# Performance work log

Measured on AMD Instinct MI355X. Metric: run time of the kernel, lower is better.

Reference implementation:

```python
import jax, jax.numpy as jnp
import numpy as np

B, T, D, H = 8, 4096, 1024, 1024


def setup_inputs() -> dict:
    key = jax.random.key(0)
    ks = jax.random.split(key, 8)
    s = 1.0 / np.sqrt(D)
    x = jax.random.normal(ks[0], (B, T, D), dtype=jnp.float32)
    Wq = jax.random.uniform(ks[1], (H, D), jnp.float32, -s, s)
    bq = jax.random.uniform(ks[2], (H,), jnp.float32, -s, s)
    Wk = jax.random.uniform(ks[3], (H, D), jnp.float32, -s, s)
    bk = jax.random.uniform(ks[4], (H,), jnp.float32, -s, s)
    Wv = jax.random.uniform(ks[5], (H, D), jnp.float32, -s, s)
    bv = jax.random.uniform(ks[6], (H,), jnp.float32, -s, s)
    wbias = jax.random.uniform(ks[7], (H,), jnp.float32, 0.0, 1.0)  # torch.rand
    return {"x": x, "Wq": Wq, "bq": bq, "Wk": Wk, "bk": bk, "Wv": Wv, "bv": bv, "wbias": wbias}


def reference(x, Wq, bq, Wk, bk, Wv, bv, wbias):
    # Q, K, V: [B, T, H]
    Q = jnp.einsum('btd,hd->bth', x, Wq) + bq
    K = jnp.einsum('btd,hd->bth', x, Wk) + bk
    V = jnp.einsum('btd,hd->bth', x, Wv) + bv
    Q_sig = jax.nn.sigmoid(Q)
    numer = jnp.exp(K + wbias)            # [B, T, H]
    denom = numer.sum(axis=0)             # [T, H] (faithful: sum over batch axis)
    weighted = (numer * V).sum(axis=0) / denom  # [T, H]
    Yt = Q_sig * weighted                 # broadcast -> [B, T, H]
    return Yt  # to_out is Identity since dim == hidden_dim
```

## Files before the change

### kernel.cpp

```cpp
#include <hip/hip_runtime.h>
#include <hip/hip_bf16.h>

#define B_ 8
#define T_ 4096
#define D_ 1024
#define H_ 1024

typedef __attribute__((ext_vector_type(8))) short short8;
typedef __attribute__((ext_vector_type(4))) float floatx4;

#define GLOAD16(gptr, lptr) \
  __builtin_amdgcn_global_load_lds((const __attribute__((address_space(1))) void*)(gptr), \
                                   (__attribute__((address_space(3))) void*)(lptr), 16, 0, 0)

__device__ __forceinline__ ushort f2b(float f) {
  unsigned x = __builtin_bit_cast(unsigned, f);
  unsigned r = (x + 0x7fffu + ((x >> 16) & 1u)) >> 16;
  return (ushort)r;
}

__global__ void cvt_kernel(const float* __restrict__ in, ushort* __restrict__ out, int n) {
  int idx = blockIdx.x * blockDim.x + threadIdx.x;
  int stride = gridDim.x * blockDim.x;
  for (long i = (long)idx * 8; i < n; i += (long)stride * 8) {
    const float4 f0 = *(const float4*)(in + i);
    const float4 f1 = *(const float4*)(in + i + 4);
    union { ushort u[8]; uint4 v; } r;
    r.u[0] = f2b(f0.x); r.u[1] = f2b(f0.y); r.u[2] = f2b(f0.z); r.u[3] = f2b(f0.w);
    r.u[4] = f2b(f1.x); r.u[5] = f2b(f1.y); r.u[6] = f2b(f1.z); r.u[7] = f2b(f1.w);
    *(uint4*)(out + i) = r.v;
  }
}

__global__ __launch_bounds__(512, 2) void kv_kernel(
    const ushort* __restrict__ xb, const ushort* __restrict__ Wkb,
    const ushort* __restrict__ Wvb, const float* __restrict__ bk,
    const float* __restrict__ bv, const float* __restrict__ wbias,
    float* __restrict__ weighted) {
  extern __shared__ ushort lds[];
  ushort* const AsB = lds;
  ushort* const KsB = lds + 49152;
  ushort* const VsB = lds + 61440;

  const int tid = threadIdx.x;
  const int lane = tid & 63;
  const int w = tid >> 6;
  const int wrow = w >> 1;
  const int wcol = w & 1;
  const int t0 = blockIdx.x * 256;
  const int h0 = blockIdx.y * 64;

  const int srow = tid >> 3;
  const int swz = (tid & 7) ^ ((tid >> 3) & 7);

  const int arow = wrow * 64 + (lane & 15);
  const int bcol = wcol * 32 + (lane & 15);
  const int cs0 = (lane >> 4) ^ (lane & 7);
  const int cs1 = ((lane >> 4) + 4) ^ (lane & 7);

  float wbc[2], bkc[2], bvc[2];
#pragma unroll
  for (int n = 0; n < 2; ++n) {
    int h = h0 + wcol * 32 + n * 16 + (lane & 15);
    wbc[n] = wbias[h];
    bkc[n] = bk[h];
    bvc[n] = bv[h];
  }

  const ushort* xsb = xb + (size_t)(t0 + srow) * D_ + swz * 8;
  const ushort* ksb = Wkb + (size_t)(h0 + srow) * D_ + swz * 8;
  const ushort* vsb = Wvb + (size_t)(h0 + srow) * D_ + swz * 8;

  auto stage = [&](int p, int nb) {
    const int b = p >> 4;
    const int kt = (p & 15) << 6;
    const ushort* xs = xsb + (size_t)b * (T_ * D_) + kt;
    ushort* Ab = AsB + nb * 16384;
#pragma unroll
    for (int it = 0; it < 4; ++it)
      GLOAD16(xs + (size_t)(it * 64) * D_, Ab + (it * 512 + tid) * 8);
    GLOAD16(ksb + kt, KsB + nb * 4096 + tid * 8);
    GLOAD16(vsb + kt, VsB + nb * 4096 + tid * 8);
  };

  floatx4 accK[4][2] = {};
  floatx4 accV[4][2] = {};
  floatx4 sumN[4][2] = {};
  floatx4 sumWV[4][2] = {};

  stage(0, 0);
  stage(1, 1);
  asm volatile("s_waitcnt vmcnt(6)" ::: "memory");
  __builtin_amdgcn_s_barrier();

  int cur = 0, stg = 2;
  for (int p = 0; p < 128; ++p) {
    if (p < 126) stage(p + 2, stg);

    const ushort* Ac = AsB + cur * 16384;
    const ushort* Kc = KsB + cur * 4096;
    const ushort* Vc = VsB + cur * 4096;
#pragma unroll
    for (int s = 0; s < 2; ++s) {
      const int cs = s ? cs1 : cs0;
      short8 a[4], kb2[2], vb2[2];
#pragma unroll
      for (int m = 0; m < 4; ++m)
        a[m] = *(const short8*)&Ac[(arow + m * 16) * 64 + cs * 8];
#pragma unroll
      for (int n = 0; n < 2; ++n) {
        kb2[n] = *(const short8*)&Kc[(bcol + n * 16) * 64 + cs * 8];
        vb2[n] = *(const short8*)&Vc[(bcol + n * 16) * 64 + cs * 8];
      }
      __builtin_amdgcn_s_setprio(1);
#pragma unroll
      for (int m = 0; m < 4; ++m)
#pragma unroll
        for (int n = 0; n < 2; ++n) {
          accK[m][n] = __builtin_amdgcn_mfma_f32_16x16x32_bf16(a[m], kb2[n], accK[m][n], 0, 0, 0);
          accV[m][n] = __builtin_amdgcn_mfma_f32_16x16x32_bf16(a[m], vb2[n], accV[m][n], 0, 0, 0);
        }
      __builtin_amdgcn_s_setprio(0);
    }

    if ((p & 15) == 15) {
#pragma unroll
      for (int m = 0; m < 4; ++m)
#pragma unroll
        for (int n = 0; n < 2; ++n) {
#pragma unroll
          for (int r = 0; r < 4; ++r) {
            float nmr = __expf(accK[m][n][r] + bkc[n] + wbc[n]);
            sumN[m][n][r] += nmr;
            sumWV[m][n][r] += nmr * (accV[m][n][r] + bvc[n]);
          }
          accK[m][n] = floatx4{0.f, 0.f, 0.f, 0.f};
          accV[m][n] = floatx4{0.f, 0.f, 0.f, 0.f};
        }
    }

    if (p < 126) { asm volatile("s_waitcnt vmcnt(6)" ::: "memory"); }
    else         { asm volatile("s_waitcnt vmcnt(0)" ::: "memory"); }
    __builtin_amdgcn_s_barrier();
    cur = (cur == 2) ? 0 : cur + 1;
    stg = (stg == 2) ? 0 : stg + 1;
  }

#pragma unroll
  for (int m = 0; m < 4; ++m)
#pragma unroll
    for (int n = 0; n < 2; ++n)
#pragma unroll
      for (int r = 0; r < 4; ++r) {
        int t = t0 + wrow * 64 + m * 16 + (lane >> 4) * 4 + r;
        int h = h0 + wcol * 32 + n * 16 + (lane & 15);
        weighted[(size_t)t * H_ + h] = sumWV[m][n][r] / sumN[m][n][r];
      }
}

__global__ __launch_bounds__(512, 2) void q_kernel(
    const ushort* __restrict__ xb, const ushort* __restrict__ Wqb,
    const float* __restrict__ bq, const float* __restrict__ weighted,
    float* __restrict__ out) {
  extern __shared__ ushort lds[];
  ushort* const AsB = lds;
  ushort* const BsB = lds + 24576;

  const int tid = threadIdx.x;
  const int lane = tid & 63;
  const int w = tid >> 6;
  const int wrow = w >> 1;
  const int wcol = w & 1;
  const int R0 = blockIdx.x * 256;
  const int h0 = blockIdx.y * 128;

  const int srow = tid >> 2;
  const int sq = (tid & 3) ^ ((tid >> 3) & 3);

  const int arow = wrow * 64 + (lane & 15);
  const int brow = wcol * 64 + (lane & 15);
  const int cq = (lane >> 4) ^ (((lane & 15) >> 1) & 3);

  const ushort* xsrc = xb + (size_t)(R0 + srow) * D_ + sq * 8;
  const ushort* wsrc = Wqb + (size_t)(h0 + srow) * D_ + sq * 8;

  auto stage = [&](int kt, int nb) {
    GLOAD16(xsrc + kt, AsB + nb * 8192 + tid * 8);
    GLOAD16(xsrc + (size_t)128 * D_ + kt, AsB + nb * 8192 + (tid + 512) * 8);
    GLOAD16(wsrc + kt, BsB + nb * 4096 + tid * 8);
  };

  floatx4 acc[4][4] = {};

  stage(0, 0);
  stage(32, 1);
  asm volatile("s_waitcnt vmcnt(3)" ::: "memory");
  __builtin_amdgcn_s_barrier();

  int cur = 0, stg = 2;
  for (int it = 0; it < 32; ++it) {
    if (it < 30) stage((it + 2) * 32, stg);

    const ushort* Ac = AsB + cur * 8192;
    const ushort* Bc = BsB + cur * 4096;
    short8 a[4], bb[4];
#pragma unroll
    for (int m = 0; m < 4; ++m)
      a[m] = *(const short8*)&Ac[(arow + m * 16) * 32 + cq * 8];
#pragma unroll
    for (int n = 0; n < 4; ++n)
      bb[n] = *(const short8*)&Bc[(brow + n * 16) * 32 + cq * 8];
    __builtin_amdgcn_s_setprio(1);
#pragma unroll
    for (int m = 0; m < 4; ++m)
#pragma unroll
      for (int n = 0; n < 4; ++n)
        acc[m][n] = __builtin_amdgcn_mfma_f32_16x16x32_bf16(a[m], bb[n], acc[m][n], 0, 0, 0);
    __builtin_amdgcn_s_setprio(0);

    if (it < 30) { asm volatile("s_waitcnt vmcnt(3)" ::: "memory"); }
    else         { asm volatile("s_waitcnt vmcnt(0)" ::: "memory"); }
    __builtin_amdgcn_s_barrier();
    cur = (cur == 2) ? 0 : cur + 1;
    stg = (stg == 2) ? 0 : stg + 1;
  }

  float bqc[4];
#pragma unroll
  for (int n = 0; n < 4; ++n)
    bqc[n] = bq[h0 + wcol * 64 + n * 16 + (lane & 15)];

#pragma unroll
  for (int m = 0; m < 4; ++m)
#pragma unroll
    for (int n = 0; n < 4; ++n)
#pragma unroll
      for (int r = 0; r < 4; ++r) {
        int row = R0 + wrow * 64 + m * 16 + (lane >> 4) * 4 + r;
        int t = row & (T_ - 1);
        int h = h0 + wcol * 64 + n * 16 + (lane & 15);
        float q = acc[m][n][r] + bqc[n];
        float sig = 1.f / (1.f + __expf(-q));
        out[(size_t)row * H_ + h] = sig * weighted[(size_t)t * H_ + h];
      }
}

extern "C" void kernel_launch(void* const* d_in, const int* in_sizes, int n_in,
                              void* d_out, int out_size, void* d_ws, size_t ws_size,
                              hipStream_t stream) {
  (void)in_sizes; (void)n_in; (void)out_size; (void)ws_size;
  const float* x = (const float*)d_in[0];
  const float* Wq = (const float*)d_in[1];
  const float* bq = (const float*)d_in[2];
  const float* Wk = (const float*)d_in[3];
  const float* bk = (const float*)d_in[4];
  const float* Wv = (const float*)d_in[5];
  const float* bv = (const float*)d_in[6];
  const float* wbias = (const float*)d_in[7];
  float* out = (float*)d_out;

  char* ws = (char*)d_ws;
  const size_t XN = (size_t)B_ * T_ * D_;
  const size_t WN = (size_t)H_ * D_;
  ushort* xb  = (ushort*)ws;
  ushort* Wqb = (ushort*)(ws + XN * 2);
  ushort* Wkb = Wqb + WN;
  ushort* Wvb = Wkb + WN;
  float* weighted = (float*)(ws + XN * 2 + 3 * WN * 2);

  (void)hipFuncSetAttribute((const void*)kv_kernel,
                            hipFuncAttributeMaxDynamicSharedMemorySize, 147456);
  (void)hipFuncSetAttribute((const void*)q_kernel,
                            hipFuncAttributeMaxDynamicSharedMemorySize, 73728);

  cvt_kernel<<<2048, 256, 0, stream>>>(x, xb, (int)XN);
  cvt_kernel<<<512, 256, 0, stream>>>(Wq, Wqb, (int)WN);
  cvt_kernel<<<512, 256, 0, stream>>>(Wk, Wkb, (int)WN);
  cvt_kernel<<<512, 256, 0, stream>>>(Wv, Wvb, (int)WN);

  kv_kernel<<<dim3(T_ / 256, H_ / 64), 512, 147456, stream>>>(xb, Wkb, Wvb, bk, bv, wbias, weighted);
  q_kernel<<<dim3((B_ * T_) / 256, H_ / 128), 512, 73728, stream>>>(xb, Wqb, bq, weighted, out);
}
```

Baseline: 285.0 us.

## Split LDS prefetch into halves interleaved with MFMA sub-steps; widen Q-GEMM K tile

```diff
diff --git a/kernel.cpp b/kernel.cpp
--- a/kernel.cpp
+++ b/kernel.cpp
@@ -71,16 +71,20 @@
   const ushort* ksb = Wkb + (size_t)(h0 + srow) * D_ + swz * 8;
   const ushort* vsb = Wvb + (size_t)(h0 + srow) * D_ + swz * 8;
 
-  auto stage = [&](int p, int nb) {
+  auto stage_half = [&](int p, int nb, int half) {
     const int b = p >> 4;
     const int kt = (p & 15) << 6;
     const ushort* xs = xsb + (size_t)b * (T_ * D_) + kt;
     ushort* Ab = AsB + nb * 16384;
-#pragma unroll
-    for (int it = 0; it < 4; ++it)
-      GLOAD16(xs + (size_t)(it * 64) * D_, Ab + (it * 512 + tid) * 8);
-    GLOAD16(ksb + kt, KsB + nb * 4096 + tid * 8);
-    GLOAD16(vsb + kt, VsB + nb * 4096 + tid * 8);
+    if (half == 0) {
+      GLOAD16(xs, Ab + tid * 8);
+      GLOAD16(xs + (size_t)64 * D_, Ab + (512 + tid) * 8);
+      GLOAD16(ksb + kt, KsB + nb * 4096 + tid * 8);
+    } else {
+      GLOAD16(xs + (size_t)128 * D_, Ab + (1024 + tid) * 8);
+      GLOAD16(xs + (size_t)192 * D_, Ab + (1536 + tid) * 8);
+      GLOAD16(vsb + kt, VsB + nb * 4096 + tid * 8);
+    }
   };
 
   floatx4 accK[4][2] = {};
@@ -88,30 +92,57 @@
   floatx4 sumN[4][2] = {};
   floatx4 sumWV[4][2] = {};
 
-  stage(0, 0);
-  stage(1, 1);
+  stage_half(0, 0, 0); stage_half(0, 0, 1);
+  stage_half(1, 1, 0); stage_half(1, 1, 1);
   asm volatile("s_waitcnt vmcnt(6)" ::: "memory");
   __builtin_amdgcn_s_barrier();
 
   int cur = 0, stg = 2;
   for (int p = 0; p < 128; ++p) {
-    if (p < 126) stage(p + 2, stg);
-
     const ushort* Ac = AsB + cur * 16384;
     const ushort* Kc = KsB + cur * 4096;
     const ushort* Vc = VsB + cur * 4096;
-#pragma unroll
-    for (int s = 0; s < 2; ++s) {
-      const int cs = s ? cs1 : cs0;
+
+    {
       short8 a[4], kb2[2], vb2[2];
 #pragma unroll
       for (int m = 0; m < 4; ++m)
-        a[m] = *(const short8*)&Ac[(arow + m * 16) * 64 + cs * 8];
+        a[m] = *(const short8*)&Ac[(arow + m * 16) * 64 + cs0 * 8];
 #pragma unroll
       for (int n = 0; n < 2; ++n) {
-        kb2[n] = *(const short8*)&Kc[(bcol + n * 16) * 64 + cs * 8];
-        vb2[n] = *(const short8*)&Vc[(bcol + n * 16) * 64 + cs * 8];
+        kb2[n] = *(const short8*)&Kc[(bcol + n * 16) * 64 + cs0 * 8];
+        vb2[n] = *(const short8*)&Vc[(bcol + n * 16) * 64 + cs0 * 8];
       }
+      if (p < 126) stage_half(p + 2, stg, 0);
+      __builtin_amdgcn_s_barrier();
+      asm volatile("s_waitcnt lgkmcnt(0)" ::: "memory");
+      __builtin_amdgcn_sched_barrier(0);
+      __builtin_amdgcn_s_setprio(1);
+#pragma unroll
+      for (int m = 0; m < 4; ++m)
+#pragma unroll
+        for (int n = 0; n < 2; ++n) {
+          accK[m][n] = __builtin_amdgcn_mfma_f32_16x16x32_bf16(a[m], kb2[n], accK[m][n], 0, 0, 0);
+          accV[m][n] = __builtin_amdgcn_mfma_f32_16x16x32_bf16(a[m], vb2[n], accV[m][n], 0, 0, 0);
+        }
+      __builtin_amdgcn_s_setprio(0);
+      __builtin_amdgcn_s_barrier();
+    }
+
+    {
+      short8 a[4], kb2[2], vb2[2];
+#pragma unroll
+      for (int m = 0; m < 4; ++m)
+        a[m] = *(const short8*)&Ac[(arow + m * 16) * 64 + cs1 * 8];
+#pragma unroll
+      for (int n = 0; n < 2; ++n) {
+        kb2[n] = *(const short8*)&Kc[(bcol + n * 16) * 64 + cs1 * 8];
+        vb2[n] = *(const short8*)&Vc[(bcol + n * 16) * 64 + cs1 * 8];
+      }
+      if (p < 126) stage_half(p + 2, stg, 1);
+      __builtin_amdgcn_s_barrier();
+      asm volatile("s_waitcnt lgkmcnt(0)" ::: "memory");
+      __builtin_amdgcn_sched_barrier(0);
       __builtin_amdgcn_s_setprio(1);
 #pragma unroll
       for (int m = 0; m < 4; ++m)
@@ -164,7 +195,7 @@
     float* __restrict__ out) {
   extern __shared__ ushort lds[];
   ushort* const AsB = lds;
-  ushort* const BsB = lds + 24576;
+  ushort* const BsB = lds + 49152;
 
   const int tid = threadIdx.x;
   const int lane = tid & 63;
@@ -174,51 +205,87 @@
   const int R0 = blockIdx.x * 256;
   const int h0 = blockIdx.y * 128;
 
-  const int srow = tid >> 2;
-  const int sq = (tid & 3) ^ ((tid >> 3) & 3);
+  const int srow = tid >> 3;
+  const int swz = (tid & 7) ^ ((tid >> 3) & 7);
 
   const int arow = wrow * 64 + (lane & 15);
   const int brow = wcol * 64 + (lane & 15);
-  const int cq = (lane >> 4) ^ (((lane & 15) >> 1) & 3);
-
-  const ushort* xsrc = xb + (size_t)(R0 + srow) * D_ + sq * 8;
-  const ushort* wsrc = Wqb + (size_t)(h0 + srow) * D_ + sq * 8;
-
-  auto stage = [&](int kt, int nb) {
-    GLOAD16(xsrc + kt, AsB + nb * 8192 + tid * 8);
-    GLOAD16(xsrc + (size_t)128 * D_ + kt, AsB + nb * 8192 + (tid + 512) * 8);
-    GLOAD16(wsrc + kt, BsB + nb * 4096 + tid * 8);
+  const int cs0 = (lane >> 4) ^ (lane & 7);
+  const int cs1 = ((lane >> 4) + 4) ^ (lane & 7);
+
+  const ushort* xsrc = xb + (size_t)(R0 + srow) * D_ + swz * 8;
+  const ushort* wsrc = Wqb + (size_t)(h0 + srow) * D_ + swz * 8;
+
+  auto stage_half = [&](int kt, int nb, int half) {
+    ushort* Ab = AsB + nb * 16384;
+    ushort* Bb = BsB + nb * 8192;
+    if (half == 0) {
+      GLOAD16(xsrc + kt, Ab + tid * 8);
+      GLOAD16(xsrc + kt + (size_t)64 * D_, Ab + (512 + tid) * 8);
+      GLOAD16(wsrc + kt, Bb + tid * 8);
+    } else {
+      GLOAD16(xsrc + kt + (size_t)128 * D_, Ab + (1024 + tid) * 8);
+      GLOAD16(xsrc + kt + (size_t)192 * D_, Ab + (1536 + tid) * 8);
+      GLOAD16(wsrc + kt + (size_t)64 * D_, Bb + (512 + tid) * 8);
+    }
   };
 
   floatx4 acc[4][4] = {};
 
-  stage(0, 0);
-  stage(32, 1);
-  asm volatile("s_waitcnt vmcnt(3)" ::: "memory");
+  stage_half(0, 0, 0); stage_half(0, 0, 1);
+  stage_half(64, 1, 0); stage_half(64, 1, 1);
+  asm volatile("s_waitcnt vmcnt(6)" ::: "memory");
   __builtin_amdgcn_s_barrier();
 
   int cur = 0, stg = 2;
-  for (int it = 0; it < 32; ++it) {
-    if (it < 30) stage((it + 2) * 32, stg);
-
-    const ushort* Ac = AsB + cur * 8192;
-    const ushort* Bc = BsB + cur * 4096;
-    short8 a[4], bb[4];
-#pragma unroll
-    for (int m = 0; m < 4; ++m)
-      a[m] = *(const short8*)&Ac[(arow + m * 16) * 32 + cq * 8];
-#pragma unroll
-    for (int n = 0; n < 4; ++n)
-      bb[n] = *(const short8*)&Bc[(brow + n * 16) * 32 + cq * 8];
-    __builtin_amdgcn_s_setprio(1);
-#pragma unroll
-    for (int m = 0; m < 4; ++m)
+  for (int it = 0; it < 16; ++it) {
+    const ushort* Ac = AsB + cur * 16384;
+    const ushort* Bc = BsB + cur * 8192;
+
+    {
+      short8 a[4], bb[4];
+#pragma unroll
+      for (int m = 0; m < 4; ++m)
+        a[m] = *(const short8*)&Ac[(arow + m * 16) * 64 + cs0 * 8];
 #pragma unroll
       for (int n = 0; n < 4; ++n)
-        acc[m][n] = __builtin_amdgcn_mfma_f32_16x16x32_bf16(a[m], bb[n], acc[m][n], 0, 0, 0);
-    __builtin_amdgcn_s_setprio(0);
-
-    if (it < 30) { asm volatile("s_waitcnt vmcnt(3)" ::: "memory"); }
+        bb[n] = *(const short8*)&Bc[(brow + n * 16) * 64 + cs0 * 8];
+      if (it < 14) stage_half((it + 2) * 64, stg, 0);
+      __builtin_amdgcn_s_barrier();
+      asm volatile("s_waitcnt lgkmcnt(0)" ::: "memory");
+      __builtin_amdgcn_sched_barrier(0);
+      __builtin_amdgcn_s_setprio(1);
+#pragma unroll
+      for (int m = 0; m < 4; ++m)
+#pragma unroll
+        for (int n = 0; n < 4; ++n)
+          acc[m][n] = __builtin_amdgcn_mfma_f32_16x16x32_bf16(a[m], bb[n], acc[m][n], 0, 0, 0);
+      __builtin_amdgcn_s_setprio(0);
+      __builtin_amdgcn_s_barrier();
+    }
+
+    {
+      short8 a[4], bb[4];
+#pragma unroll
+      for (int m = 0; m < 4; ++m)
+        a[m] = *(const short8*)&Ac[(arow + m * 16) * 64 + cs1 * 8];
+#pragma unroll
+      for (int n = 0; n < 4; ++n)
+        bb[n] = *(const short8*)&Bc[(brow + n * 16) * 64 + cs1 * 8];
+      if (it < 14) stage_half((it + 2) * 64, stg, 1);
+      __builtin_amdgcn_s_barrier();
+      asm volatile("s_waitcnt lgkmcnt(0)" ::: "memory");
+      __builtin_amdgcn_sched_barrier(0);
+      __builtin_amdgcn_s_setprio(1);
+#pragma unroll
+      for (int m = 0; m < 4; ++m)
+#pragma unroll
+        for (int n = 0; n < 4; ++n)
+          acc[m][n] = __builtin_amdgcn_mfma_f32_16x16x32_bf16(a[m], bb[n], acc[m][n], 0, 0, 0);
+      __builtin_amdgcn_s_setprio(0);
+    }
+
+    if (it < 14) { asm volatile("s_waitcnt vmcnt(6)" ::: "memory"); }
     else         { asm volatile("s_waitcnt vmcnt(0)" ::: "memory"); }
     __builtin_amdgcn_s_barrier();
     cur = (cur == 2) ? 0 : cur + 1;
@@ -271,7 +338,7 @@
   (void)hipFuncSetAttribute((const void*)kv_kernel,
                             hipFuncAttributeMaxDynamicSharedMemorySize, 147456);
   (void)hipFuncSetAttribute((const void*)q_kernel,
-                            hipFuncAttributeMaxDynamicSharedMemorySize, 73728);
+                            hipFuncAttributeMaxDynamicSharedMemorySize, 147456);
 
   cvt_kernel<<<2048, 256, 0, stream>>>(x, xb, (int)XN);
   cvt_kernel<<<512, 256, 0, stream>>>(Wq, Wqb, (int)WN);
@@ -279,5 +346,5 @@
   cvt_kernel<<<512, 256, 0, stream>>>(Wv, Wvb, (int)WN);
 
   kv_kernel<<<dim3(T_ / 256, H_ / 64), 512, 147456, stream>>>(xb, Wkb, Wvb, bk, bv, wbias, weighted);
-  q_kernel<<<dim3((B_ * T_) / 256, H_ / 128), 512, 73728, stream>>>(xb, Wqb, bq, weighted, out);
-}
+  q_kernel<<<dim3((B_ * T_) / 256, H_ / 128), 512, 147456, stream>>>(xb, Wqb, bq, weighted, out);
+}
```

Result: no change. 287.0 us (+0.7%).
